# Kernel optimization log

Hardware: AMD Instinct MI355X
Metric: run time of the kernel (lower is better)

Reference implementation:

```python
import jax, jax.numpy as jnp
import numpy as np

SIGMA = 2.0
RADIUS = 2.5


def setup_inputs() -> dict:
    key = jax.random.key(0)
    k0, k1, k2, k3, k4, k5 = jax.random.split(key, 6)
    Nq, Ns, K, Kp, Cin, Cout = 50000, 50000, 32, 15, 64, 64
    s_feats = jax.random.uniform(k0, (Ns, Cin), dtype=jnp.float32)
    q_points = jax.random.normal(k1, (Nq, 3), dtype=jnp.float32)
    s_points = jax.random.normal(k2, (Ns, 3), dtype=jnp.float32)
    neighbor_indices = jax.random.randint(k3, (Nq, K), 0, Ns)
    # rigid kernel point dispositions within the kernel radius (load_kernels stand-in)
    kernel_points = jax.random.uniform(k4, (Kp, 3), minval=-1.0, maxval=1.0,
                                       dtype=jnp.float32) * (RADIUS * 0.66)
    # kaiming_uniform_ with a=sqrt(5) -> bound = 1/sqrt(fan_in)
    bound = 1.0 / np.sqrt(Cin)
    weights = jax.random.uniform(k5, (Kp, Cin, Cout), minval=-bound, maxval=bound,
                                 dtype=jnp.float32)
    return dict(s_feats=s_feats, q_points=q_points, s_points=s_points,
                neighbor_indices=neighbor_indices, kernel_points=kernel_points,
                weights=weights)


def reference(s_feats, q_points, s_points, neighbor_indices, kernel_points, weights):
    # pad support points with a far-away shadow point (index Ns)
    shadow_pt = jnp.full((1, s_points.shape[1]), 1e6, dtype=s_points.dtype)
    s_pts = jnp.concatenate([s_points, shadow_pt], axis=0)
    # gather neighbor coordinates, center on query points: [Nq, K, 3]
    neighbors = s_pts[neighbor_indices] - q_points[:, None, :]
    # squared distance to each kernel point: [Nq, K, Kp]
    sq_distances = jnp.sum((neighbors[:, :, None, :] - kernel_points[None, None]) ** 2,
                           axis=-1)
    # linear correlation influence, clamped at 0: [Nq, K, Kp]
    all_weights = jnp.maximum(1.0 - jnp.sqrt(sq_distances) / SIGMA, 0.0)
    # pad support features with a zero shadow feature row
    sf = jnp.concatenate([s_feats, jnp.zeros((1, s_feats.shape[1]), s_feats.dtype)],
                         axis=0)
    neighb_x = sf[neighbor_indices]  # [Nq, K, Cin]
    # aggregate neighbor features per kernel point: [Nq, Kp, Cin]
    weighted = jnp.einsum('nkp,nkc->npc', all_weights, neighb_x)
    # apply per-kernel-point weight matrices and sum over kernel points: [Nq, Cout]
    output_features = jnp.einsum('npc,pcd->nd', weighted, weights)
    # density normalization: count valid (non-shadow, positive-sum) neighbors
    neighbor_features_sum = jnp.sum(neighb_x, axis=-1)          # [Nq, K]
    neighbor_num = jnp.sum(neighbor_features_sum > 0.0, axis=-1)  # [Nq]
    neighbor_num = jnp.maximum(neighbor_num, 1)
    return output_features / neighbor_num[:, None].astype(output_features.dtype)
```

## Files before the change

### kernel.cpp

```cpp
#include <hip/hip_runtime.h>
#include <hip/hip_bf16.h>

typedef __attribute__((ext_vector_type(8))) short short8;
typedef __attribute__((ext_vector_type(4))) float f32x4;

#define WT_BYTE_OFF 6400000

#define QSTRIDE   2064
#define XSLICE    4128
#define LDS_NN    33024
#define LDS_POS   33088
#define POSSTRIDE 1024
#define LDS_RED   33088
#define LDS_TOT   (33088 + 8*1024)

__device__ inline unsigned short f2bf(float x) {
    unsigned int u = __float_as_uint(x);
    unsigned int r = (u + 0x7FFFu + ((u >> 16) & 1u)) >> 16;
    return (unsigned short)r;
}

__device__ inline unsigned short f2bf_fast(float x) {
    __hip_bfloat16 b = __float2bfloat16(x);
    return *reinterpret_cast<unsigned short*>(&b);
}

__global__ void kpconv_pre(const float* __restrict__ s_feats,
                           const float* __restrict__ weights,
                           unsigned short* __restrict__ xbf,
                           unsigned short* __restrict__ wfrag) {
    int t = blockIdx.x * 256 + threadIdx.x;
    if (t < 800000) {
        int i = t * 4;
        float4 v = *(const float4*)(s_feats + i);
        ushort4 o;
        o.x = f2bf(v.x); o.y = f2bf(v.y); o.z = f2bf(v.z); o.w = f2bf(v.w);
        *(ushort4*)(xbf + i) = o;
    } else {
        int tw = t - 800000;
        if (tw < 8192) {
            const int f = tw >> 6, l = tw & 63;
            const int m = l & 15, h = l >> 4;
            const int dt = f >> 5, kh = (f >> 4) & 1, jj = f & 15;
            const int d = dt * 16 + m;
            const int pcb = (kh * 16 + jj) * 32 + 8 * h;
            ushort4 o0, o1;
            unsigned short* op0 = (unsigned short*)&o0;
            unsigned short* op1 = (unsigned short*)&o1;
            #pragma unroll
            for (int e = 0; e < 8; ++e) {
                const int pc = pcb + e;
                const int p = pc & 15, c = pc >> 4;
                const float wv = (p < 15) ? weights[(p * 64 + c) * 64 + d] : 0.0f;
                if (e < 4) op0[e] = f2bf(wv); else op1[e - 4] = f2bf(wv);
            }
            *(ushort4*)(wfrag + tw * 8) = o0;
            *(ushort4*)(wfrag + tw * 8 + 4) = o1;
        }
    }
}

__global__ __launch_bounds__(512, 6) void kpconv_main(
    const float* __restrict__ qpts, const float* __restrict__ spts,
    const int* __restrict__ nbr, const float* __restrict__ kpts,
    const unsigned short* __restrict__ xbf, const unsigned short* __restrict__ wfrag,
    float* __restrict__ out)
{
    __shared__ unsigned char lds[LDS_TOT];
    const int tid = threadIdx.x;
    const int w = tid >> 6;
    const int l = tid & 63;
    const int h = l >> 4;
    const int m = l & 15;
    const int qbase = blockIdx.x * 16;

    const int pm = (m < 15) ? m : 14;
    const float kx = kpts[pm * 3 + 0], ky = kpts[pm * 3 + 1], kz = kpts[pm * 3 + 2];

    unsigned char* xw = lds + w * XSLICE;
    unsigned char* posb = lds + LDS_POS + w * POSSTRIDE;

    const int* nbase = nbr + (qbase + 2 * w) * 32;
    const int sBoth = nbase[l];

    const float2 pxy = *(const float2*)(spts + (size_t)sBoth * 3);
    const float pz = spts[(size_t)sBoth * 3 + 2];
    f32x4 pe;
    pe[0] = pxy.x; pe[1] = pxy.y; pe[2] = pz;
    pe[3] = __builtin_fmaf(pz, pz,
            __builtin_fmaf(pxy.y, pxy.y, pxy.x * pxy.x));
    *(f32x4*)(posb + l * 16) = pe;
    asm volatile("s_waitcnt lgkmcnt(0)" ::: "memory");
    __builtin_amdgcn_sched_barrier(0);

    const int voff = l >> 3;
    int sidx[2][4];
    #pragma unroll
    for (int i = 0; i < 2; ++i)
        #pragma unroll
        for (int g = 0; g < 4; ++g)
            sidx[i][g] = nbase[32 * i + 8 * g + voff];

    int4 xv[2][4];
    #pragma unroll
    for (int i = 0; i < 2; ++i)
        #pragma unroll
        for (int g = 0; g < 4; ++g)
            xv[i][g] = *(const int4*)(xbf + (size_t)sidx[i][g] * 64 + (l & 7) * 8);

    unsigned char* wb2 = xw + (l & 7) * 512 + (l >> 3) * 2;
    const int xb2 = (l & 3) << 4;
    unsigned char* rb3 = xw + m * 64;
    const int rxb = (h ^ (m >> 3)) << 4;

    uint2 pk0[4];

    #pragma unroll
    for (int i = 0; i < 2; ++i) {
        const int ql = 2 * w + i;
        const int q = qbase + ql;

        int nn = 0;
        #pragma unroll
        for (int g = 0; g < 4; ++g) {
            const int4 v = xv[i][g];
            unsigned long long b = __ballot((v.x | v.y | v.z | v.w) != 0);
            b |= b >> 4; b |= b >> 2; b |= b >> 1;
            nn += __popcll(b & 0x0101010101010101ULL);
        }
        if (nn < 1) nn = 1;
        if (l == 0) *(int*)(lds + LDS_NN + ql * 4) = nn;

        #pragma unroll
        for (int g = 0; g < 4; ++g) {
            const unsigned short* u8 = (const unsigned short*)&xv[i][g];
            unsigned char* wg = wb2 + ((g << 4) ^ xb2);
            #pragma unroll
            for (int e = 0; e < 8; ++e)
                *(unsigned short*)(wg + e * 64) = u8[e];
        }

        const float qx = qpts[q * 3 + 0], qy = qpts[q * 3 + 1], qz = qpts[q * 3 + 2];
        const float bx = qx + kx, by = qy + ky, bz = qz + kz;
        const float n2bx = -2.0f * bx, n2by = -2.0f * by, n2bz = -2.0f * bz;
        const float bb = __builtin_fmaf(bz, bz, __builtin_fmaf(by, by, bx * bx));
        float wv[8];
        #pragma unroll
        for (int j = 0; j < 8; ++j) {
            const f32x4 pv = *(const f32x4*)(posb + i * 512 + h * 128 + j * 16);
            float t = __builtin_fmaf(pv[2], n2bz, pv[3]);
            t = __builtin_fmaf(pv[1], n2by, t);
            t = __builtin_fmaf(pv[0], n2bx, t);
            const float d2 = t + bb;
            const float s = __builtin_amdgcn_sqrtf(d2);
            wv[j] = fmaxf(__builtin_fmaf(s, -0.5f, 1.0f), 0.0f);
        }
        union { unsigned int d[4]; short8 s8; } au;
        const bool pad = (m == 15);
        #pragma unroll
        for (int jp = 0; jp < 4; ++jp) {
            const unsigned int pk = (unsigned int)f2bf_fast(wv[2 * jp]) |
                                    ((unsigned int)f2bf_fast(wv[2 * jp + 1]) << 16);
            au.d[jp] = pad ? 0u : pk;
        }

        f32x4 c3[4];
        #pragma unroll
        for (int ct = 0; ct < 4; ++ct) {
            short8 b3 = *(const short8*)(rb3 + ct * 1024 + (rxb ^ ((ct & 1) << 5)));
            f32x4 z = {0.f, 0.f, 0.f, 0.f};
            c3[ct] = __builtin_amdgcn_mfma_f32_16x16x32_bf16(au.s8, b3, z, 0, 0, 0);
        }

        #pragma unroll
        for (int ct = 0; ct < 4; ++ct) {
            uint2 pkv;
            pkv.x = (unsigned int)f2bf_fast(c3[ct][0]) | ((unsigned int)f2bf_fast(c3[ct][1]) << 16);
            pkv.y = (unsigned int)f2bf_fast(c3[ct][2]) | ((unsigned int)f2bf_fast(c3[ct][3]) << 16);
            if (i == 0) {
                pk0[ct] = pkv;
            } else {
                *(uint2*)(lds + ql * QSTRIDE + (ct * 16 + m) * 32 + h * 8) = pkv;
            }
        }
    }

    #pragma unroll
    for (int ct = 0; ct < 4; ++ct)
        *(uint2*)(lds + (2 * w) * QSTRIDE + (ct * 16 + m) * 32 + h * 8) = pk0[ct];

    __syncthreads();

    const int dt = w & 3, kh = w >> 2;
    const int d = dt * 16 + m;
    f32x4 acc0 = {0.f, 0.f, 0.f, 0.f}, acc1 = {0.f, 0.f, 0.f, 0.f};
    const unsigned char* abase = lds + m * QSTRIDE + 16 * h;
    const unsigned short* bbase = wfrag + (size_t)((dt * 2 + kh) * 16) * 512 + l * 8;
    const int k0 = kh * 16;
    #pragma unroll
    for (int j = 0; j < 8; ++j) {
        short8 a4a = *(const short8*)(abase + (k0 + j) * 64);
        short8 b4a = *(const short8*)(bbase + j * 512);
        acc0 = __builtin_amdgcn_mfma_f32_16x16x32_bf16(a4a, b4a, acc0, 0, 0, 0);
        short8 a4b = *(const short8*)(abase + (k0 + 8 + j) * 64);
        short8 b4b = *(const short8*)(bbase + (8 + j) * 512);
        acc1 = __builtin_amdgcn_mfma_f32_16x16x32_bf16(a4b, b4b, acc1, 0, 0, 0);
    }

    if (kh == 1) {
        f32x4 acc = acc0 + acc1;
        *(f32x4*)(lds + LDS_RED + dt * 1024 + l * 16) = acc;
    }
    __syncthreads();
    if (kh == 0) {
        f32x4 part = *(const f32x4*)(lds + LDS_RED + dt * 1024 + l * 16);
        #pragma unroll
        for (int r = 0; r < 4; ++r) {
            const int qr = 4 * h + r;
            const int nn = *(const int*)(lds + LDS_NN + qr * 4);
            out[(size_t)(qbase + qr) * 64 + d] =
                (acc0[r] + acc1[r] + part[r]) * (1.0f / (float)nn);
        }
    }
}

extern "C" void kernel_launch(void* const* d_in, const int* in_sizes, int n_in,
                              void* d_out, int out_size, void* d_ws, size_t ws_size,
                              hipStream_t stream) {
    const float* s_feats = (const float*)d_in[0];
    const float* q_points = (const float*)d_in[1];
    const float* s_points = (const float*)d_in[2];
    const int* nbr = (const int*)d_in[3];
    const float* kpts = (const float*)d_in[4];
    const float* wts = (const float*)d_in[5];
    float* out = (float*)d_out;

    unsigned short* xbf = (unsigned short*)d_ws;
    unsigned short* wfrag = (unsigned short*)((char*)d_ws + WT_BYTE_OFF);

    hipLaunchKernelGGL(kpconv_pre, dim3(3157), dim3(256), 0, stream,
                       s_feats, wts, xbf, wfrag);
    hipLaunchKernelGGL(kpconv_main, dim3(3125), dim3(512), 0, stream,
                       q_points, s_points, nbr, kpts, xbf, wfrag, out);
}
```

Before: 55.27 us.

## Use ds_read_b64_tr_b16 transpose loads for neighbor features and swizzle position LDS

Replaces the scalar 16-bit scattered LDS writes that transposed neighbor features with vectorized 128-bit row-major writes, then reads MFMA B operands with the gfx950 ds_read_b64_tr_b16 transpose-load instruction. The LDS slice strides are enlarged and the position buffer is XOR-swizzled to avoid bank conflicts. This cuts many small LDS stores, at the cost of an explicit lgkmcnt wait and reliance on the exact transpose-load lane mapping, which must produce the same fragment layout as before.

```diff
diff --git a/kernel.cpp b/kernel.cpp
--- a/kernel.cpp
+++ b/kernel.cpp
@@ -3,16 +3,17 @@
 
 typedef __attribute__((ext_vector_type(8))) short short8;
 typedef __attribute__((ext_vector_type(4))) float f32x4;
+typedef __attribute__((ext_vector_type(2))) unsigned int u32x2;
 
 #define WT_BYTE_OFF 6400000
 
-#define QSTRIDE   2064
-#define XSLICE    4128
-#define LDS_NN    33024
-#define LDS_POS   33088
+#define QSTRIDE   2112
+#define XSLICE    4224
+#define LDS_NN    33792
+#define LDS_POS   33856
 #define POSSTRIDE 1024
-#define LDS_RED   33088
-#define LDS_TOT   (33088 + 8*1024)
+#define LDS_RED   33856
+#define LDS_TOT   (33856 + 8*1024)
 
 __device__ inline unsigned short f2bf(float x) {
     unsigned int u = __float_as_uint(x);
@@ -66,7 +67,7 @@
     const unsigned short* __restrict__ xbf, const unsigned short* __restrict__ wfrag,
     float* __restrict__ out)
 {
-    __shared__ unsigned char lds[LDS_TOT];
+    __shared__ __attribute__((aligned(128))) unsigned char lds[LDS_TOT];
     const int tid = threadIdx.x;
     const int w = tid >> 6;
     const int l = tid & 63;
@@ -89,7 +90,7 @@
     pe[0] = pxy.x; pe[1] = pxy.y; pe[2] = pz;
     pe[3] = __builtin_fmaf(pz, pz,
             __builtin_fmaf(pxy.y, pxy.y, pxy.x * pxy.x));
-    *(f32x4*)(posb + l * 16) = pe;
+    *(f32x4*)(posb + ((l ^ ((l >> 3) & 7)) << 4)) = pe;
     asm volatile("s_waitcnt lgkmcnt(0)" ::: "memory");
     __builtin_amdgcn_sched_barrier(0);
 
@@ -108,10 +109,10 @@
         for (int g = 0; g < 4; ++g)
             xv[i][g] = *(const int4*)(xbf + (size_t)sidx[i][g] * 64 + (l & 7) * 8);
 
-    unsigned char* wb2 = xw + (l & 7) * 512 + (l >> 3) * 2;
-    const int xb2 = (l & 3) << 4;
-    unsigned char* rb3 = xw + m * 64;
-    const int rxb = (h ^ (m >> 3)) << 4;
+    const int lo7 = l & 7;
+    unsigned char* xwl = xw + ((l >> 5) * 512 + (lo7 >> 1) * 128 +
+                               ((l >> 3) & 3) * 32 + (lo7 & 1) * 16);
+    const unsigned xrd = (unsigned)(size_t)xw + h * 1024 + m * 8;
 
     uint2 pk0[4];
 
@@ -132,22 +133,29 @@
         if (l == 0) *(int*)(lds + LDS_NN + ql * 4) = nn;
 
         #pragma unroll
-        for (int g = 0; g < 4; ++g) {
-            const unsigned short* u8 = (const unsigned short*)&xv[i][g];
-            unsigned char* wg = wb2 + ((g << 4) ^ xb2);
-            #pragma unroll
-            for (int e = 0; e < 8; ++e)
-                *(unsigned short*)(wg + e * 64) = u8[e];
+        for (int g = 0; g < 4; ++g)
+            *(int4*)(xwl + g * 1024) = xv[i][g];
+
+        u32x2 tA[4], tB[4];
+        #pragma unroll
+        for (int ct = 0; ct < 4; ++ct) {
+            const unsigned xa = xrd + ct * 128;
+            asm volatile("ds_read_b64_tr_b16 %0, %2\n\t"
+                         "ds_read_b64_tr_b16 %1, %2 offset:512"
+                         : "=&v"(tA[ct]), "=&v"(tB[ct])
+                         : "v"(xa) : "memory");
         }
 
         const float qx = qpts[q * 3 + 0], qy = qpts[q * 3 + 1], qz = qpts[q * 3 + 2];
         const float bx = qx + kx, by = qy + ky, bz = qz + kz;
         const float n2bx = -2.0f * bx, n2by = -2.0f * by, n2bz = -2.0f * bz;
         const float bb = __builtin_fmaf(bz, bz, __builtin_fmaf(by, by, bx * bx));
+        const int hsw = 4 * i + h;
         float wv[8];
         #pragma unroll
         for (int j = 0; j < 8; ++j) {
-            const f32x4 pv = *(const f32x4*)(posb + i * 512 + h * 128 + j * 16);
+            const f32x4 pv = *(const f32x4*)(posb + i * 512 + h * 128 +
+                                             ((j ^ hsw) << 4));
             float t = __builtin_fmaf(pv[2], n2bz, pv[3]);
             t = __builtin_fmaf(pv[1], n2by, t);
             t = __builtin_fmaf(pv[0], n2bx, t);
@@ -164,12 +172,17 @@
             au.d[jp] = pad ? 0u : pk;
         }
 
+        asm volatile("s_waitcnt lgkmcnt(0)" ::: "memory");
+        __builtin_amdgcn_sched_barrier(0);
+
         f32x4 c3[4];
         #pragma unroll
         for (int ct = 0; ct < 4; ++ct) {
-            short8 b3 = *(const short8*)(rb3 + ct * 1024 + (rxb ^ ((ct & 1) << 5)));
+            union { unsigned int d[4]; short8 s8; } bu;
+            bu.d[0] = tA[ct][0]; bu.d[1] = tA[ct][1];
+            bu.d[2] = tB[ct][0]; bu.d[3] = tB[ct][1];
             f32x4 z = {0.f, 0.f, 0.f, 0.f};
-            c3[ct] = __builtin_amdgcn_mfma_f32_16x16x32_bf16(au.s8, b3, z, 0, 0, 0);
+            c3[ct] = __builtin_amdgcn_mfma_f32_16x16x32_bf16(au.s8, bu.s8, z, 0, 0, 0);
         }
 
         #pragma unroll
```

Result: slower. 59.16 us (+7.0%).
